# Kernel tuning notes

Measured on AMD Instinct MI355X. Metric: run time of the kernel, lower is better.

Reference implementation:

```python
import jax, jax.numpy as jnp
import numpy as np

B, C, H, W = 16, 64, 64, 64  # z_e shape; C == embedding_dim
K = 1024                     # num_embeddings
COMMITMENT_COST = 0.25
EPS = 1e-5


def setup_inputs() -> dict:
    key = jax.random.key(0)
    k1, k2 = jax.random.split(key)
    z_e = jax.random.normal(k1, (B, C, H, W), dtype=jnp.float32)
    # codebook init ~ U(-1/D, 1/D) as in the torch module
    emb_w = jax.random.uniform(k2, (K, C), dtype=jnp.float32, minval=-1.0 / C, maxval=1.0 / C)
    return {"z_e": z_e, "emb_w": emb_w}


def reference(z_e, emb_w):
    orig_dtype = z_e.dtype
    b, c, h, w = z_e.shape
    z = z_e.astype(jnp.float32)
    # per-channel std over (batch, h, w); computed under no_grad in torch -> stop_gradient
    std = jax.lax.stop_gradient(
        jnp.clip(jnp.std(z, axis=(0, 2, 3), keepdims=True, ddof=1), EPS, None)
    )
    z = z / std                                        # [b,c,h,w]
    zf = z.transpose(0, 2, 3, 1).reshape(-1, c)        # [N, c]
    ew = emb_w.astype(jnp.float32)                     # [K, c]
    # squared euclidean distances: ||z||^2 - 2 z.e + ||e||^2  -> [N, K]
    d = (
        jnp.sum(zf * zf, axis=1, keepdims=True)
        - 2.0 * (zf @ ew.T)
        + jnp.sum(ew * ew, axis=1)
    )
    idx = jnp.argmin(d, axis=1)                        # [N]
    z_q = ew[idx].reshape(b, h, w, c).transpose(0, 3, 1, 2)  # [b,c,h,w]
    z_sg = jax.lax.stop_gradient(z)
    commitment = COMMITMENT_COST * jnp.mean((z_sg - z_q) ** 2)
    codebook = jnp.mean((z_sg - z_q) ** 2)             # eval-mode codebook loss
    vq_loss = commitment + codebook
    z_q_st = (z + jax.lax.stop_gradient(z_q - z)).astype(orig_dtype)
    n_tokens = idx.shape[0]
    counts = jnp.zeros((K,), dtype=jnp.float32).at[idx].add(1.0)
    avg_probs = counts / n_tokens
    perplexity = jnp.exp(-jnp.sum(avg_probs * jnp.log(jnp.clip(avg_probs, 1e-10, None))))
    indices = idx.reshape(b, h, w)
    return z_q_st, vq_loss, perplexity, indices
```

## Files before the change

kernel.cpp:

```cpp
#include <hip/hip_runtime.h>
#include <math.h>
#include <float.h>

#define HW 4096
#define CHW 262144
#define NTOK 65536
#define NELEM 4194304

#define WS_LOSS 0
#define WS_STD  512
#define WS_EE   576
#define WS_ETG  1600

__device__ __forceinline__ void gload_lds16(const float* g, float* l) {
  __builtin_amdgcn_global_load_lds(
      (const __attribute__((address_space(1))) unsigned int*)g,
      (__attribute__((address_space(3))) unsigned int*)l, 16, 0, 0);
}

__global__ __launch_bounds__(1024) void k_pre(const float* __restrict__ z,
                                              const float* __restrict__ emb,
                                              float* __restrict__ stdv,
                                              float* __restrict__ etg,
                                              float* __restrict__ eeg) {
  __shared__ double rs[16], rs2[16];
  __shared__ float T[64][65];
  int tid = threadIdx.x;
  int blk = blockIdx.x;
  if (blk < 64) {
    int c = blk;
    double s = 0.0, s2 = 0.0;
    const float* base = z + c * HW;
    #pragma unroll 4
    for (int jj = 0; jj < 16; ++jj) {
      int f = tid + (jj << 10);
      int b = f >> 10, off4 = f & 1023;
      float4 v = *(const float4*)(base + (size_t)b * CHW + (off4 << 2));
      s  += (double)v.x + (double)v.y + (double)v.z + (double)v.w;
      s2 += (double)v.x * v.x + (double)v.y * v.y + (double)v.z * v.z + (double)v.w * v.w;
    }
    for (int o = 32; o > 0; o >>= 1) {
      s += __shfl_down(s, o, 64);
      s2 += __shfl_down(s2, o, 64);
    }
    int wv = tid >> 6, ln = tid & 63;
    if (ln == 0) { rs[wv] = s; rs2[wv] = s2; }
    __syncthreads();
    if (tid == 0) {
      double S = 0.0, S2 = 0.0;
      #pragma unroll
      for (int w = 0; w < 16; ++w) { S += rs[w]; S2 += rs2[w]; }
      const double N = (double)NTOK;
      double var = (S2 - S * S / N) / (N - 1.0);
      float sd = (float)sqrt(var);
      stdv[c] = fmaxf(sd, 1e-5f);
    }
  } else {
    int k0 = (blk - 64) << 6;
    {
      int code = tid >> 4, c4 = tid & 15;
      float4 v = *(const float4*)(emb + (size_t)((k0 + code) << 6) + (c4 << 2));
      T[code][(c4 << 2) + 0] = v.x;
      T[code][(c4 << 2) + 1] = v.y;
      T[code][(c4 << 2) + 2] = v.z;
      T[code][(c4 << 2) + 3] = v.w;
    }
    __syncthreads();
    {
      int c = tid >> 4, k4 = tid & 15;
      float4 v = make_float4(T[(k4 << 2) + 0][c], T[(k4 << 2) + 1][c],
                             T[(k4 << 2) + 2][c], T[(k4 << 2) + 3][c]);
      *(float4*)(etg + c * 1024 + k0 + (k4 << 2)) = v;
    }
    if (tid < 64) {
      const float* er = emb + (size_t)((k0 + tid) << 6);
      float s = 0.f;
      #pragma unroll
      for (int c = 0; c < 64; ++c) s = fmaf(er[c], er[c], s);
      eeg[k0 + tid] = s;
    }
  }
}

#define FMA8(ii, zc) \
  acc[ii].x = fmaf(zc, ea.x, acc[ii].x); \
  acc[ii].y = fmaf(zc, ea.y, acc[ii].y); \
  acc[ii].z = fmaf(zc, ea.z, acc[ii].z); \
  acc[ii].w = fmaf(zc, ea.w, acc[ii].w);

__global__ __launch_bounds__(256, 3) void k_vq(
    const float* __restrict__ z_e, const float* __restrict__ emb,
    const float* __restrict__ stdv, const float* __restrict__ eeg,
    const float* __restrict__ etg,
    float* __restrict__ out_zq, float* __restrict__ out_idx,
    float* __restrict__ loss_part) {
  __shared__ float zt[64 * 128];
  __shared__ float et[64 * 64];
  __shared__ float eetS[64];
  __shared__ float zzt[128];
  __shared__ float sstd[64];
  __shared__ float rbd[2 * 128];
  __shared__ int   rbk[2 * 128];
  __shared__ int   skf[128];
  __shared__ float sred[4];

  int tid = threadIdx.x;
  int lane = tid & 63;
  int wv = tid >> 6;
  int blk = blockIdx.x;
  int b = blk >> 5;
  int s0 = (blk & 31) << 7;

  if (tid < 64) sstd[tid] = stdv[tid];
  __syncthreads();

  const float* zbase = z_e + (size_t)b * CHW + s0;
  #pragma unroll
  for (int jj = 0; jj < 8; ++jj) {
    int f = tid + (jj << 8);
    int c = f >> 5, t4 = f & 31;
    float4 v = *(const float4*)(zbase + (size_t)c * HW + (t4 << 2));
    float sd = sstd[c];
    v.x /= sd; v.y /= sd; v.z /= sd; v.w /= sd;
    *(float4*)&zt[(c << 7) + (t4 << 2)] = v;
  }
  __syncthreads();

  if (tid < 128) {
    float a = 0.f;
    #pragma unroll
    for (int c = 0; c < 64; ++c) { float v = zt[(c << 7) + tid]; a = fmaf(v, v, a); }
    zzt[tid] = a;
  }
  __syncthreads();

  int toff = ((wv >> 1) << 6) + ((lane >> 3) << 3);
  int kloc = ((wv & 1) << 5) + ((lane & 7) << 2);
  int tq4 = toff >> 2;
  int kq4 = kloc >> 2;

  float zzr[8];
  #pragma unroll
  for (int ii = 0; ii < 8; ++ii) zzr[ii] = zzt[toff + ii];

  float bd[8]; int bk[8];
  #pragma unroll
  for (int ii = 0; ii < 8; ++ii) { bd[ii] = FLT_MAX; bk[ii] = 0; }

  int c0 = tid >> 4;
  int k16 = (tid & 15) << 2;
  const float* gbase = etg + c0 * 1024 + k16;
  float* lbase = et + (c0 << 6) + k16;

  for (int tile = 0; tile < 16; ++tile) {
    __syncthreads();
    {
      const float* gsrc = gbase + (tile << 6);
      #pragma unroll
      for (int jj = 0; jj < 4; ++jj)
        gload_lds16(gsrc + jj * 16384, lbase + jj * 1024);
      if (tid < 64) eetS[tid] = eeg[(tile << 6) + tid];
    }
    __syncthreads();

    float4 acc[8];
    #pragma unroll
    for (int ii = 0; ii < 8; ++ii) acc[ii] = make_float4(0.f, 0.f, 0.f, 0.f);

    #pragma unroll 8
    for (int c = 0; c < 64; ++c) {
      float4 ea = ((const float4*)et)[(c << 4) + kq4];
      float4 za = ((const float4*)zt)[(c << 5) + tq4];
      float4 zb = ((const float4*)zt)[(c << 5) + tq4 + 1];
      FMA8(0, za.x) FMA8(1, za.y) FMA8(2, za.z) FMA8(3, za.w)
      FMA8(4, zb.x) FMA8(5, zb.y) FMA8(6, zb.z) FMA8(7, zb.w)
    }

    int kb = (tile << 6) + kloc;
    float e0 = eetS[kloc], e1 = eetS[kloc + 1];
    float e2 = eetS[kloc + 2], e3 = eetS[kloc + 3];
    #pragma unroll
    for (int ii = 0; ii < 8; ++ii) {
      float z2 = zzr[ii];
      float dd0 = (z2 - 2.0f * acc[ii].x) + e0;
      float dd1 = (z2 - 2.0f * acc[ii].y) + e1;
      float dd2 = (z2 - 2.0f * acc[ii].z) + e2;
      float dd3 = (z2 - 2.0f * acc[ii].w) + e3;
      if (dd0 < bd[ii]) { bd[ii] = dd0; bk[ii] = kb; }
      if (dd1 < bd[ii]) { bd[ii] = dd1; bk[ii] = kb + 1; }
      if (dd2 < bd[ii]) { bd[ii] = dd2; bk[ii] = kb + 2; }
      if (dd3 < bd[ii]) { bd[ii] = dd3; bk[ii] = kb + 3; }
    }
  }

  #pragma unroll
  for (int m = 1; m <= 4; m <<= 1) {
    #pragma unroll
    for (int ii = 0; ii < 8; ++ii) {
      float od = __shfl_xor(bd[ii], m, 64);
      int   ok = __shfl_xor(bk[ii], m, 64);
      if (od < bd[ii] || (od == bd[ii] && ok < bk[ii])) { bd[ii] = od; bk[ii] = ok; }
    }
  }
  if ((lane & 7) == 0) {
    int base = ((wv & 1) << 7) + toff;
    #pragma unroll
    for (int ii = 0; ii < 8; ++ii) { rbd[base + ii] = bd[ii]; rbk[base + ii] = bk[ii]; }
  }
  __syncthreads();

  if (tid < 128) {
    float d0 = rbd[tid];       int k0 = rbk[tid];
    float d1 = rbd[128 + tid]; int k1 = rbk[128 + tid];
    int kb2 = (d1 < d0 || (d1 == d0 && k1 < k0)) ? k1 : k0;
    skf[tid] = kb2;
    out_idx[(blk << 7) + tid] = (float)kb2;
  }
  __syncthreads();

  int t = tid & 127;
  int ch = tid >> 7;
  int kq = skf[t];
  const float* eq = emb + (size_t)(kq << 6) + (ch << 5);
  float lsum = 0.f;
  float* ob = out_zq + (size_t)b * CHW + s0 + t;
  #pragma unroll
  for (int jj = 0; jj < 32; ++jj) {
    int c = (ch << 5) + jj;
    float zv = zt[(c << 7) + t];
    float e = eq[jj];
    float df = zv - e;
    lsum = fmaf(df, df, lsum);
    ob[(size_t)c * HW] = zv + (e - zv);
  }
  for (int o = 32; o > 0; o >>= 1) lsum += __shfl_down(lsum, o, 64);
  if (lane == 0) sred[wv] = lsum;
  __syncthreads();
  if (tid == 0) loss_part[blk] = sred[0] + sred[1] + sred[2] + sred[3];
}

__global__ __launch_bounds__(1024) void k_post(const float* __restrict__ loss_part,
                                               const float* __restrict__ out_idx,
                                               float* __restrict__ out_scalars) {
  __shared__ int hist[1024];
  __shared__ double rl[16], rh[16];
  int tid = threadIdx.x;
  hist[tid] = 0;
  __syncthreads();
  const float2* idx2 = (const float2*)out_idx;
  #pragma unroll
  for (int jj = 0; jj < 32; ++jj) {
    float2 v = idx2[tid + (jj << 10)];
    atomicAdd(&hist[(int)v.x], 1);
    atomicAdd(&hist[(int)v.y], 1);
  }
  __syncthreads();
  double ls = 0.0;
  if (tid < 512) ls = (double)loss_part[tid];
  float p = (float)hist[tid] * (1.0f / 65536.0f);
  float lg = logf(fmaxf(p, 1e-10f));
  double hs = (double)(p * lg);
  for (int o = 32; o > 0; o >>= 1) {
    ls += __shfl_down(ls, o, 64);
    hs += __shfl_down(hs, o, 64);
  }
  int wv = tid >> 6, ln = tid & 63;
  if (ln == 0) { rl[wv] = ls; rh[wv] = hs; }
  __syncthreads();
  if (tid == 0) {
    double L = 0.0, Hn = 0.0;
    #pragma unroll
    for (int w = 0; w < 16; ++w) { L += rl[w]; Hn += rh[w]; }
    float m = (float)(L / (double)NELEM);
    out_scalars[0] = 0.25f * m + m;
    out_scalars[1] = expf((float)(-Hn));
  }
}

extern "C" void kernel_launch(void* const* d_in, const int* in_sizes, int n_in,
                              void* d_out, int out_size, void* d_ws, size_t ws_size,
                              hipStream_t stream) {
  const float* z_e = (const float*)d_in[0];
  const float* emb = (const float*)d_in[1];
  float* ws = (float*)d_ws;
  float* loss_part = ws + WS_LOSS;
  float* stdv = ws + WS_STD;
  float* eeg = ws + WS_EE;
  float* etg = ws + WS_ETG;

  float* out = (float*)d_out;
  float* out_zq = out;
  float* out_scalars = out + NELEM;
  float* out_idx = out + NELEM + 2;

  k_pre<<<80, 1024, 0, stream>>>(z_e, emb, stdv, etg, eeg);
  k_vq<<<512, 256, 0, stream>>>(z_e, emb, stdv, eeg, etg, out_zq, out_idx, loss_part);
  k_post<<<1, 1024, 0, stream>>>(loss_part, out_idx, out_scalars);
}
```

Measured before the change: 206.6 us.

## Read codebook directly from global memory and fuse post-reduction into last block

The distance loop no longer stages codebook tiles in LDS with barriers. Each thread now reads 8 codebook columns straight from global/L2 memory and keeps 64 accumulators over 8 passes. The separate single-block post kernel is removed: the last VQ block to finish, detected with a global atomic counter, builds the histogram and writes the loss and perplexity scalars. This removes per-tile barriers and one kernel launch, but it adds register pressure and uncached global reads in the inner loop, and the final reduction now runs with only 256 threads.

```diff
diff --git a/kernel.cpp b/kernel.cpp
--- a/kernel.cpp
+++ b/kernel.cpp
@@ -11,22 +11,19 @@
 #define WS_STD  512
 #define WS_EE   576
 #define WS_ETG  1600
-
-__device__ __forceinline__ void gload_lds16(const float* g, float* l) {
-  __builtin_amdgcn_global_load_lds(
-      (const __attribute__((address_space(1))) unsigned int*)g,
-      (__attribute__((address_space(3))) unsigned int*)l, 16, 0, 0);
-}
+#define WS_DONE 67136
 
 __global__ __launch_bounds__(1024) void k_pre(const float* __restrict__ z,
                                               const float* __restrict__ emb,
                                               float* __restrict__ stdv,
                                               float* __restrict__ etg,
-                                              float* __restrict__ eeg) {
+                                              float* __restrict__ eeg,
+                                              int* __restrict__ done) {
   __shared__ double rs[16], rs2[16];
   __shared__ float T[64][65];
   int tid = threadIdx.x;
   int blk = blockIdx.x;
+  if (blk == 0 && tid == 0) *done = 0;
   if (blk < 64) {
     int c = blk;
     double s = 0.0, s2 = 0.0;
@@ -82,27 +79,33 @@
   }
 }
 
-#define FMA8(ii, zc) \
-  acc[ii].x = fmaf(zc, ea.x, acc[ii].x); \
-  acc[ii].y = fmaf(zc, ea.y, acc[ii].y); \
-  acc[ii].z = fmaf(zc, ea.z, acc[ii].z); \
-  acc[ii].w = fmaf(zc, ea.w, acc[ii].w);
+#define STEP8(i, zc) \
+  acc0[i].x = fmaf(zc, ea.x, acc0[i].x); \
+  acc0[i].y = fmaf(zc, ea.y, acc0[i].y); \
+  acc0[i].z = fmaf(zc, ea.z, acc0[i].z); \
+  acc0[i].w = fmaf(zc, ea.w, acc0[i].w); \
+  acc1[i].x = fmaf(zc, eb.x, acc1[i].x); \
+  acc1[i].y = fmaf(zc, eb.y, acc1[i].y); \
+  acc1[i].z = fmaf(zc, eb.z, acc1[i].z); \
+  acc1[i].w = fmaf(zc, eb.w, acc1[i].w);
 
 __global__ __launch_bounds__(256, 3) void k_vq(
     const float* __restrict__ z_e, const float* __restrict__ emb,
     const float* __restrict__ stdv, const float* __restrict__ eeg,
     const float* __restrict__ etg,
     float* __restrict__ out_zq, float* __restrict__ out_idx,
-    float* __restrict__ loss_part) {
+    float* __restrict__ loss_part, int* __restrict__ done,
+    float* __restrict__ out_scalars) {
   __shared__ float zt[64 * 128];
-  __shared__ float et[64 * 64];
-  __shared__ float eetS[64];
   __shared__ float zzt[128];
   __shared__ float sstd[64];
-  __shared__ float rbd[2 * 128];
-  __shared__ int   rbk[2 * 128];
+  __shared__ float rbd[2][128];
+  __shared__ int   rbk[2][128];
   __shared__ int   skf[128];
   __shared__ float sred[4];
+  __shared__ int   hist[1024];
+  __shared__ int   lastFlag;
+  __shared__ double rl[4], rh[4];
 
   int tid = threadIdx.x;
   int lane = tid & 63;
@@ -134,62 +137,54 @@
   }
   __syncthreads();
 
-  int toff = ((wv >> 1) << 6) + ((lane >> 3) << 3);
-  int kloc = ((wv & 1) << 5) + ((lane & 7) << 2);
-  int tq4 = toff >> 2;
-  int kq4 = kloc >> 2;
+  int tg = lane >> 3, cg = lane & 7;
+  int wt = wv >> 1, wc = wv & 1;
+  int tbase = wt * 64 + tg * 8;
+  const float4* zp = (const float4*)&zt[tbase];
 
   float zzr[8];
   #pragma unroll
-  for (int ii = 0; ii < 8; ++ii) zzr[ii] = zzt[toff + ii];
+  for (int ii = 0; ii < 8; ++ii) zzr[ii] = zzt[tbase + ii];
 
   float bd[8]; int bk[8];
   #pragma unroll
   for (int ii = 0; ii < 8; ++ii) { bd[ii] = FLT_MAX; bk[ii] = 0; }
 
-  int c0 = tid >> 4;
-  int k16 = (tid & 15) << 2;
-  const float* gbase = etg + c0 * 1024 + k16;
-  float* lbase = et + (c0 << 6) + k16;
-
-  for (int tile = 0; tile < 16; ++tile) {
-    __syncthreads();
-    {
-      const float* gsrc = gbase + (tile << 6);
-      #pragma unroll
-      for (int jj = 0; jj < 4; ++jj)
-        gload_lds16(gsrc + jj * 16384, lbase + jj * 1024);
-      if (tid < 64) eetS[tid] = eeg[(tile << 6) + tid];
-    }
-    __syncthreads();
-
-    float4 acc[8];
-    #pragma unroll
-    for (int ii = 0; ii < 8; ++ii) acc[ii] = make_float4(0.f, 0.f, 0.f, 0.f);
-
-    #pragma unroll 8
+  for (int pass = 0; pass < 8; ++pass) {
+    int kk = (pass << 7) + (wc << 6) + (cg << 3);
+    const float* ep = etg + kk;
+
+    float4 acc0[8], acc1[8];
+    #pragma unroll
+    for (int ii = 0; ii < 8; ++ii) {
+      acc0[ii] = make_float4(0.f, 0.f, 0.f, 0.f);
+      acc1[ii] = make_float4(0.f, 0.f, 0.f, 0.f);
+    }
+
+    #pragma unroll 4
     for (int c = 0; c < 64; ++c) {
-      float4 ea = ((const float4*)et)[(c << 4) + kq4];
-      float4 za = ((const float4*)zt)[(c << 5) + tq4];
-      float4 zb = ((const float4*)zt)[(c << 5) + tq4 + 1];
-      FMA8(0, za.x) FMA8(1, za.y) FMA8(2, za.z) FMA8(3, za.w)
-      FMA8(4, zb.x) FMA8(5, zb.y) FMA8(6, zb.z) FMA8(7, zb.w)
-    }
-
-    int kb = (tile << 6) + kloc;
-    float e0 = eetS[kloc], e1 = eetS[kloc + 1];
-    float e2 = eetS[kloc + 2], e3 = eetS[kloc + 3];
+      float4 ea = *(const float4*)ep;
+      float4 eb = *(const float4*)(ep + 4);
+      float4 za = zp[c << 5];
+      float4 zb = zp[(c << 5) + 1];
+      STEP8(0, za.x) STEP8(1, za.y) STEP8(2, za.z) STEP8(3, za.w)
+      STEP8(4, zb.x) STEP8(5, zb.y) STEP8(6, zb.z) STEP8(7, zb.w)
+      ep += 1024;
+    }
+
+    float4 eea = *(const float4*)(eeg + kk);
+    float4 eeb = *(const float4*)(eeg + kk + 4);
+    float eev[8] = {eea.x, eea.y, eea.z, eea.w, eeb.x, eeb.y, eeb.z, eeb.w};
     #pragma unroll
     for (int ii = 0; ii < 8; ++ii) {
       float z2 = zzr[ii];
-      float dd0 = (z2 - 2.0f * acc[ii].x) + e0;
-      float dd1 = (z2 - 2.0f * acc[ii].y) + e1;
-      float dd2 = (z2 - 2.0f * acc[ii].z) + e2;
-      float dd3 = (z2 - 2.0f * acc[ii].w) + e3;
-      if (dd0 < bd[ii]) { bd[ii] = dd0; bk[ii] = kb; }
-      if (dd1 < bd[ii]) { bd[ii] = dd1; bk[ii] = kb + 1; }
-      if (dd2 < bd[ii]) { bd[ii] = dd2; bk[ii] = kb + 2; }
-      if (dd3 < bd[ii]) { bd[ii] = dd3; bk[ii] = kb + 3; }
+      float av[8] = {acc0[ii].x, acc0[ii].y, acc0[ii].z, acc0[ii].w,
+                     acc1[ii].x, acc1[ii].y, acc1[ii].z, acc1[ii].w};
+      #pragma unroll
+      for (int jj = 0; jj < 8; ++jj) {
+        float dd = (z2 - 2.0f * av[jj]) + eev[jj];
+        if (dd < bd[ii]) { bd[ii] = dd; bk[ii] = kk + jj; }
+      }
     }
   }
 
@@ -202,75 +197,80 @@
       if (od < bd[ii] || (od == bd[ii] && ok < bk[ii])) { bd[ii] = od; bk[ii] = ok; }
     }
   }
-  if ((lane & 7) == 0) {
-    int base = ((wv & 1) << 7) + toff;
-    #pragma unroll
-    for (int ii = 0; ii < 8; ++ii) { rbd[base + ii] = bd[ii]; rbk[base + ii] = bk[ii]; }
+  if (cg == 0) {
+    #pragma unroll
+    for (int ii = 0; ii < 8; ++ii) { rbd[wc][tbase + ii] = bd[ii]; rbk[wc][tbase + ii] = bk[ii]; }
   }
   __syncthreads();
 
   if (tid < 128) {
-    float d0 = rbd[tid];       int k0 = rbk[tid];
-    float d1 = rbd[128 + tid]; int k1 = rbk[128 + tid];
+    float d0 = rbd[0][tid]; int k0 = rbk[0][tid];
+    float d1 = rbd[1][tid]; int k1 = rbk[1][tid];
     int kb2 = (d1 < d0 || (d1 == d0 && k1 < k0)) ? k1 : k0;
     skf[tid] = kb2;
     out_idx[(blk << 7) + tid] = (float)kb2;
   }
   __syncthreads();
 
-  int t = tid & 127;
-  int ch = tid >> 7;
-  int kq = skf[t];
-  const float* eq = emb + (size_t)(kq << 6) + (ch << 5);
-  float lsum = 0.f;
-  float* ob = out_zq + (size_t)b * CHW + s0 + t;
-  #pragma unroll
-  for (int jj = 0; jj < 32; ++jj) {
-    int c = (ch << 5) + jj;
-    float zv = zt[(c << 7) + t];
-    float e = eq[jj];
-    float df = zv - e;
-    lsum = fmaf(df, df, lsum);
-    ob[(size_t)c * HW] = zv + (e - zv);
-  }
-  for (int o = 32; o > 0; o >>= 1) lsum += __shfl_down(lsum, o, 64);
-  if (lane == 0) sred[wv] = lsum;
-  __syncthreads();
-  if (tid == 0) loss_part[blk] = sred[0] + sred[1] + sred[2] + sred[3];
-}
-
-__global__ __launch_bounds__(1024) void k_post(const float* __restrict__ loss_part,
-                                               const float* __restrict__ out_idx,
-                                               float* __restrict__ out_scalars) {
-  __shared__ int hist[1024];
-  __shared__ double rl[16], rh[16];
-  int tid = threadIdx.x;
-  hist[tid] = 0;
-  __syncthreads();
-  const float2* idx2 = (const float2*)out_idx;
-  #pragma unroll
-  for (int jj = 0; jj < 32; ++jj) {
-    float2 v = idx2[tid + (jj << 10)];
-    atomicAdd(&hist[(int)v.x], 1);
-    atomicAdd(&hist[(int)v.y], 1);
-  }
-  __syncthreads();
-  double ls = 0.0;
-  if (tid < 512) ls = (double)loss_part[tid];
-  float p = (float)hist[tid] * (1.0f / 65536.0f);
-  float lg = logf(fmaxf(p, 1e-10f));
-  double hs = (double)(p * lg);
+  {
+    int t = tid & 127;
+    int ch = tid >> 7;
+    int kq = skf[t];
+    const float* eq = emb + (size_t)(kq << 6) + (ch << 5);
+    float lsum = 0.f;
+    float* ob = out_zq + (size_t)b * CHW + s0 + t;
+    #pragma unroll
+    for (int jj = 0; jj < 32; ++jj) {
+      int c = (ch << 5) + jj;
+      float zv = zt[(c << 7) + t];
+      float e = eq[jj];
+      float df = zv - e;
+      lsum = fmaf(df, df, lsum);
+      ob[(size_t)c * HW] = zv + (e - zv);
+    }
+    for (int o = 32; o > 0; o >>= 1) lsum += __shfl_down(lsum, o, 64);
+    if (lane == 0) sred[wv] = lsum;
+  }
+  __syncthreads();
+
+  if (tid == 0) {
+    loss_part[blk] = sred[0] + sred[1] + sred[2] + sred[3];
+    __threadfence();
+    int prev = atomicAdd(done, 1);
+    lastFlag = (prev == 511);
+  }
+  __syncthreads();
+  if (!lastFlag) return;
+
+  #pragma unroll
+  for (int jj = 0; jj < 4; ++jj) hist[tid + (jj << 8)] = 0;
+  __syncthreads();
+  {
+    const float2* idx2 = (const float2*)out_idx;
+    for (int i = tid; i < NTOK / 2; i += 256) {
+      float2 v = idx2[i];
+      atomicAdd(&hist[(int)v.x], 1);
+      atomicAdd(&hist[(int)v.y], 1);
+    }
+  }
+  __syncthreads();
+  double ls = (double)loss_part[tid] + (double)loss_part[tid + 256];
+  double hs = 0.0;
+  #pragma unroll
+  for (int jj = 0; jj < 4; ++jj) {
+    float p = (float)hist[tid + (jj << 8)] * (1.0f / 65536.0f);
+    float lg = logf(fmaxf(p, 1e-10f));
+    hs += (double)(p * lg);
+  }
   for (int o = 32; o > 0; o >>= 1) {
     ls += __shfl_down(ls, o, 64);
     hs += __shfl_down(hs, o, 64);
   }
-  int wv = tid >> 6, ln = tid & 63;
-  if (ln == 0) { rl[wv] = ls; rh[wv] = hs; }
+  if (lane == 0) { rl[wv] = ls; rh[wv] = hs; }
   __syncthreads();
   if (tid == 0) {
-    double L = 0.0, Hn = 0.0;
-    #pragma unroll
-    for (int w = 0; w < 16; ++w) { L += rl[w]; Hn += rh[w]; }
+    double L = rl[0] + rl[1] + rl[2] + rl[3];
+    double Hn = rh[0] + rh[1] + rh[2] + rh[3];
     float m = (float)(L / (double)NELEM);
     out_scalars[0] = 0.25f * m + m;
     out_scalars[1] = expf((float)(-Hn));
@@ -287,13 +287,14 @@
   float* stdv = ws + WS_STD;
   float* eeg = ws + WS_EE;
   float* etg = ws + WS_ETG;
+  int* done = (int*)(ws + WS_DONE);
 
   float* out = (float*)d_out;
   float* out_zq = out;
   float* out_scalars = out + NELEM;
   float* out_idx = out + NELEM + 2;
 
-  k_pre<<<80, 1024, 0, stream>>>(z_e, emb, stdv, etg, eeg);
-  k_vq<<<512, 256, 0, stream>>>(z_e, emb, stdv, eeg, etg, out_zq, out_idx, loss_part);
-  k_post<<<1, 1024, 0, stream>>>(loss_part, out_idx, out_scalars);
+  k_pre<<<80, 1024, 0, stream>>>(z_e, emb, stdv, etg, eeg, done);
+  k_vq<<<512, 256, 0, stream>>>(z_e, emb, stdv, eeg, etg, out_zq, out_idx,
+                                loss_part, done, out_scalars);
 }
```

Result: slower. 299.9 us (+45.2%).

## Compute VQ distances with split-bf16 MFMA and exact fp32 fallback for near-ties

Applied to the files above, without the earlier changes.

Replaces the fp32 FMA distance GEMM with bf16 MFMA, splitting each value into high and low bf16 parts so three cross products approximate fp32 accuracy. Each token tracks its best and second-best distance, and tokens whose margin falls below a threshold are recomputed exactly in fp32 against the full codebook. The z tile is no longer kept as fp32 in LDS, so the output stage re-reads z_e from global memory. This trades extra global reads, fallback work and lower occupancy (launch bounds 3 to 2) for much higher matrix throughput.

```diff
diff --git a/kernel.cpp b/kernel.cpp
--- a/kernel.cpp
+++ b/kernel.cpp
@@ -10,21 +10,28 @@
 #define WS_LOSS 0
 #define WS_STD  512
 #define WS_EE   576
-#define WS_ETG  1600
-
-__device__ __forceinline__ void gload_lds16(const float* g, float* l) {
-  __builtin_amdgcn_global_load_lds(
-      (const __attribute__((address_space(1))) unsigned int*)g,
-      (__attribute__((address_space(3))) unsigned int*)l, 16, 0, 0);
+#define WS_E2   1600
+
+#define EPSM 2.0e-3f
+
+typedef __attribute__((ext_vector_type(8))) short bf16x8;
+typedef __attribute__((ext_vector_type(4))) float f32x4;
+
+__device__ __forceinline__ unsigned short f2bf(float x) {
+  unsigned u = __float_as_uint(x);
+  u += 0x7FFFu + ((u >> 16) & 1u);
+  return (unsigned short)(u >> 16);
+}
+__device__ __forceinline__ float bf2f(unsigned short h) {
+  return __uint_as_float(((unsigned)h) << 16);
 }
 
 __global__ __launch_bounds__(1024) void k_pre(const float* __restrict__ z,
                                               const float* __restrict__ emb,
                                               float* __restrict__ stdv,
-                                              float* __restrict__ etg,
+                                              unsigned short* __restrict__ e2g,
                                               float* __restrict__ eeg) {
   __shared__ double rs[16], rs2[16];
-  __shared__ float T[64][65];
   int tid = threadIdx.x;
   int blk = blockIdx.x;
   if (blk < 64) {
@@ -60,17 +67,14 @@
     {
       int code = tid >> 4, c4 = tid & 15;
       float4 v = *(const float4*)(emb + (size_t)((k0 + code) << 6) + (c4 << 2));
-      T[code][(c4 << 2) + 0] = v.x;
-      T[code][(c4 << 2) + 1] = v.y;
-      T[code][(c4 << 2) + 2] = v.z;
-      T[code][(c4 << 2) + 3] = v.w;
-    }
-    __syncthreads();
-    {
-      int c = tid >> 4, k4 = tid & 15;
-      float4 v = make_float4(T[(k4 << 2) + 0][c], T[(k4 << 2) + 1][c],
-                             T[(k4 << 2) + 2][c], T[(k4 << 2) + 3][c]);
-      *(float4*)(etg + c * 1024 + k0 + (k4 << 2)) = v;
+      unsigned short h0 = f2bf(v.x), h1 = f2bf(v.y), h2 = f2bf(v.z), h3 = f2bf(v.w);
+      unsigned short l0 = f2bf(v.x - bf2f(h0)), l1 = f2bf(v.y - bf2f(h1));
+      unsigned short l2 = f2bf(v.z - bf2f(h2)), l3 = f2bf(v.w - bf2f(h3));
+      unsigned short* row = e2g + (size_t)(k0 + code) * 128;
+      *(uint2*)(row + (c4 << 2)) =
+          make_uint2((unsigned)h0 | ((unsigned)h1 << 16), (unsigned)h2 | ((unsigned)h3 << 16));
+      *(uint2*)(row + 64 + (c4 << 2)) =
+          make_uint2((unsigned)l0 | ((unsigned)l1 << 16), (unsigned)l2 | ((unsigned)l3 << 16));
     }
     if (tid < 64) {
       const float* er = emb + (size_t)((k0 + tid) << 6);
@@ -82,26 +86,22 @@
   }
 }
 
-#define FMA8(ii, zc) \
-  acc[ii].x = fmaf(zc, ea.x, acc[ii].x); \
-  acc[ii].y = fmaf(zc, ea.y, acc[ii].y); \
-  acc[ii].z = fmaf(zc, ea.z, acc[ii].z); \
-  acc[ii].w = fmaf(zc, ea.w, acc[ii].w);
-
-__global__ __launch_bounds__(256, 3) void k_vq(
+__global__ __launch_bounds__(256, 2) void k_vq(
     const float* __restrict__ z_e, const float* __restrict__ emb,
     const float* __restrict__ stdv, const float* __restrict__ eeg,
-    const float* __restrict__ etg,
+    const unsigned short* __restrict__ e2g,
     float* __restrict__ out_zq, float* __restrict__ out_idx,
     float* __restrict__ loss_part) {
-  __shared__ float zt[64 * 128];
-  __shared__ float et[64 * 64];
-  __shared__ float eetS[64];
-  __shared__ float zzt[128];
+  __shared__ unsigned short Abuf[128 * 136];
+  __shared__ unsigned short Bt[128 * 136];
+  __shared__ float eeS[1024];
   __shared__ float sstd[64];
-  __shared__ float rbd[2 * 128];
-  __shared__ int   rbk[2 * 128];
+  __shared__ float mbd[2][128];
+  __shared__ float msec[2][128];
+  __shared__ int   mbk[2][128];
   __shared__ int   skf[128];
+  __shared__ int   ambList[128];
+  __shared__ int   ambN;
   __shared__ float sred[4];
 
   int tid = threadIdx.x;
@@ -112,129 +112,188 @@
   int s0 = (blk & 31) << 7;
 
   if (tid < 64) sstd[tid] = stdv[tid];
-  __syncthreads();
-
-  const float* zbase = z_e + (size_t)b * CHW + s0;
   #pragma unroll
-  for (int jj = 0; jj < 8; ++jj) {
-    int f = tid + (jj << 8);
-    int c = f >> 5, t4 = f & 31;
-    float4 v = *(const float4*)(zbase + (size_t)c * HW + (t4 << 2));
-    float sd = sstd[c];
-    v.x /= sd; v.y /= sd; v.z /= sd; v.w /= sd;
-    *(float4*)&zt[(c << 7) + (t4 << 2)] = v;
-  }
-  __syncthreads();
-
-  if (tid < 128) {
-    float a = 0.f;
-    #pragma unroll
-    for (int c = 0; c < 64; ++c) { float v = zt[(c << 7) + tid]; a = fmaf(v, v, a); }
-    zzt[tid] = a;
-  }
-  __syncthreads();
-
-  int toff = ((wv >> 1) << 6) + ((lane >> 3) << 3);
-  int kloc = ((wv & 1) << 5) + ((lane & 7) << 2);
-  int tq4 = toff >> 2;
-  int kq4 = kloc >> 2;
-
-  float zzr[8];
+  for (int j = 0; j < 4; ++j) eeS[tid + (j << 8)] = eeg[tid + (j << 8)];
+  if (tid == 0) ambN = 0;
+  __syncthreads();
+
+  {
+    int tok = tid & 127, sect = tid >> 7;
+    const float* zsrc = z_e + (size_t)b * CHW + (size_t)(sect << 5) * HW + s0 + tok;
+    unsigned hw[16], lw[16];
+    #pragma unroll
+    for (int cc = 0; cc < 32; ++cc) {
+      float v = zsrc[(size_t)cc * HW] / sstd[(sect << 5) + cc];
+      unsigned short h = f2bf(v);
+      unsigned short l = f2bf(v - bf2f(h));
+      if (cc & 1) { hw[cc >> 1] |= ((unsigned)h) << 16; lw[cc >> 1] |= ((unsigned)l) << 16; }
+      else        { hw[cc >> 1] = h;                    lw[cc >> 1] = l; }
+    }
+    unsigned short* arow = Abuf + tok * 136;
+    #pragma unroll
+    for (int q = 0; q < 4; ++q) {
+      *(uint4*)(arow + (sect << 5) + (q << 3)) =
+          make_uint4(hw[4 * q], hw[4 * q + 1], hw[4 * q + 2], hw[4 * q + 3]);
+      *(uint4*)(arow + 64 + (sect << 5) + (q << 3)) =
+          make_uint4(lw[4 * q], lw[4 * q + 1], lw[4 * q + 2], lw[4 * q + 3]);
+    }
+  }
+
+  int quad = lane >> 4, l15 = lane & 15;
+  int wt = wv >> 1, wc = wv & 1;
+
+  float bd[16], sec[16];
+  int bk[16];
   #pragma unroll
-  for (int ii = 0; ii < 8; ++ii) zzr[ii] = zzt[toff + ii];
-
-  float bd[8]; int bk[8];
-  #pragma unroll
-  for (int ii = 0; ii < 8; ++ii) { bd[ii] = FLT_MAX; bk[ii] = 0; }
-
-  int c0 = tid >> 4;
-  int k16 = (tid & 15) << 2;
-  const float* gbase = etg + c0 * 1024 + k16;
-  float* lbase = et + (c0 << 6) + k16;
-
-  for (int tile = 0; tile < 16; ++tile) {
+  for (int i = 0; i < 16; ++i) { bd[i] = FLT_MAX; sec[i] = FLT_MAX; bk[i] = 0; }
+
+  for (int ct = 0; ct < 8; ++ct) {
     __syncthreads();
     {
-      const float* gsrc = gbase + (tile << 6);
-      #pragma unroll
-      for (int jj = 0; jj < 4; ++jj)
-        gload_lds16(gsrc + jj * 16384, lbase + jj * 1024);
-      if (tid < 64) eetS[tid] = eeg[(tile << 6) + tid];
+      int code = tid >> 1, part = tid & 1;
+      const uint4* src = (const uint4*)(e2g + ((size_t)((ct << 7) + code) << 7) + (part << 6));
+      uint4* dst = (uint4*)(Bt + code * 136 + (part << 6));
+      #pragma unroll
+      for (int j = 0; j < 8; ++j) dst[j] = src[j];
     }
     __syncthreads();
 
-    float4 acc[8];
-    #pragma unroll
-    for (int ii = 0; ii < 8; ++ii) acc[ii] = make_float4(0.f, 0.f, 0.f, 0.f);
-
-    #pragma unroll 8
-    for (int c = 0; c < 64; ++c) {
-      float4 ea = ((const float4*)et)[(c << 4) + kq4];
-      float4 za = ((const float4*)zt)[(c << 5) + tq4];
-      float4 zb = ((const float4*)zt)[(c << 5) + tq4 + 1];
-      FMA8(0, za.x) FMA8(1, za.y) FMA8(2, za.z) FMA8(3, za.w)
-      FMA8(4, zb.x) FMA8(5, zb.y) FMA8(6, zb.z) FMA8(7, zb.w)
-    }
-
-    int kb = (tile << 6) + kloc;
-    float e0 = eetS[kloc], e1 = eetS[kloc + 1];
-    float e2 = eetS[kloc + 2], e3 = eetS[kloc + 3];
-    #pragma unroll
-    for (int ii = 0; ii < 8; ++ii) {
-      float z2 = zzr[ii];
-      float dd0 = (z2 - 2.0f * acc[ii].x) + e0;
-      float dd1 = (z2 - 2.0f * acc[ii].y) + e1;
-      float dd2 = (z2 - 2.0f * acc[ii].z) + e2;
-      float dd3 = (z2 - 2.0f * acc[ii].w) + e3;
-      if (dd0 < bd[ii]) { bd[ii] = dd0; bk[ii] = kb; }
-      if (dd1 < bd[ii]) { bd[ii] = dd1; bk[ii] = kb + 1; }
-      if (dd2 < bd[ii]) { bd[ii] = dd2; bk[ii] = kb + 2; }
-      if (dd3 < bd[ii]) { bd[ii] = dd3; bk[ii] = kb + 3; }
+    f32x4 acc[4][4];
+    #pragma unroll
+    for (int mt = 0; mt < 4; ++mt)
+      #pragma unroll
+      for (int nt = 0; nt < 4; ++nt) acc[mt][nt] = (f32x4)(0.f);
+
+    const int aoffs[6] = {0, 32, 64, 96, 0, 32};
+    const int boffs[6] = {0, 32, 0, 32, 64, 96};
+    #pragma unroll
+    for (int s = 0; s < 6; ++s) {
+      bf16x8 af[4], bfr[4];
+      #pragma unroll
+      for (int mt = 0; mt < 4; ++mt)
+        af[mt] = *(const bf16x8*)(Abuf + ((wt << 6) + (mt << 4) + l15) * 136 + aoffs[s] + (quad << 3));
+      #pragma unroll
+      for (int nt = 0; nt < 4; ++nt)
+        bfr[nt] = *(const bf16x8*)(Bt + ((wc << 6) + (nt << 4) + l15) * 136 + boffs[s] + (quad << 3));
+      #pragma unroll
+      for (int mt = 0; mt < 4; ++mt)
+        #pragma unroll
+        for (int nt = 0; nt < 4; ++nt)
+          acc[mt][nt] = __builtin_amdgcn_mfma_f32_16x16x32_bf16(af[mt], bfr[nt], acc[mt][nt], 0, 0, 0);
+    }
+
+    int kbase = (ct << 7) + (wc << 6);
+    #pragma unroll
+    for (int nt = 0; nt < 4; ++nt) {
+      int kcode = kbase + (nt << 4) + l15;
+      float eev = eeS[kcode];
+      #pragma unroll
+      for (int mt = 0; mt < 4; ++mt) {
+        #pragma unroll
+        for (int r = 0; r < 4; ++r) {
+          float sv = fmaf(-2.0f, acc[mt][nt][r], eev);
+          int slot = (mt << 2) + r;
+          if (sv < bd[slot]) { sec[slot] = bd[slot]; bd[slot] = sv; bk[slot] = kcode; }
+          else if (sv < sec[slot]) { sec[slot] = sv; }
+        }
+      }
     }
   }
 
   #pragma unroll
-  for (int m = 1; m <= 4; m <<= 1) {
-    #pragma unroll
-    for (int ii = 0; ii < 8; ++ii) {
-      float od = __shfl_xor(bd[ii], m, 64);
-      int   ok = __shfl_xor(bk[ii], m, 64);
-      if (od < bd[ii] || (od == bd[ii] && ok < bk[ii])) { bd[ii] = od; bk[ii] = ok; }
-    }
-  }
-  if ((lane & 7) == 0) {
-    int base = ((wv & 1) << 7) + toff;
-    #pragma unroll
-    for (int ii = 0; ii < 8; ++ii) { rbd[base + ii] = bd[ii]; rbk[base + ii] = bk[ii]; }
+  for (int m = 1; m <= 8; m <<= 1) {
+    #pragma unroll
+    for (int slot = 0; slot < 16; ++slot) {
+      float obd = __shfl_xor(bd[slot], m, 64);
+      int   obk = __shfl_xor(bk[slot], m, 64);
+      float osec = __shfl_xor(sec[slot], m, 64);
+      if (obd < bd[slot] || (obd == bd[slot] && obk < bk[slot])) {
+        sec[slot] = fminf(bd[slot], osec); bd[slot] = obd; bk[slot] = obk;
+      } else {
+        sec[slot] = fminf(sec[slot], obd);
+      }
+    }
+  }
+  if (l15 == 0) {
+    #pragma unroll
+    for (int mt = 0; mt < 4; ++mt)
+      #pragma unroll
+      for (int r = 0; r < 4; ++r) {
+        int t = (wt << 6) + (mt << 4) + (quad << 2) + r;
+        int slot = (mt << 2) + r;
+        mbd[wc][t] = bd[slot]; mbk[wc][t] = bk[slot]; msec[wc][t] = sec[slot];
+      }
   }
   __syncthreads();
 
   if (tid < 128) {
-    float d0 = rbd[tid];       int k0 = rbk[tid];
-    float d1 = rbd[128 + tid]; int k1 = rbk[128 + tid];
-    int kb2 = (d1 < d0 || (d1 == d0 && k1 < k0)) ? k1 : k0;
-    skf[tid] = kb2;
-    out_idx[(blk << 7) + tid] = (float)kb2;
-  }
-  __syncthreads();
-
-  int t = tid & 127;
-  int ch = tid >> 7;
-  int kq = skf[t];
-  const float* eq = emb + (size_t)(kq << 6) + (ch << 5);
-  float lsum = 0.f;
-  float* ob = out_zq + (size_t)b * CHW + s0 + t;
-  #pragma unroll
-  for (int jj = 0; jj < 32; ++jj) {
-    int c = (ch << 5) + jj;
-    float zv = zt[(c << 7) + t];
-    float e = eq[jj];
-    float df = zv - e;
-    lsum = fmaf(df, df, lsum);
-    ob[(size_t)c * HW] = zv + (e - zv);
-  }
-  for (int o = 32; o > 0; o >>= 1) lsum += __shfl_down(lsum, o, 64);
-  if (lane == 0) sred[wv] = lsum;
+    float b0 = mbd[0][tid], b1 = mbd[1][tid];
+    int k0 = mbk[0][tid], k1 = mbk[1][tid];
+    float fbd, fsec; int fbk;
+    if (b1 < b0 || (b1 == b0 && k1 < k0)) { fbd = b1; fbk = k1; fsec = fminf(b0, msec[1][tid]); }
+    else                                  { fbd = b0; fbk = k0; fsec = fminf(msec[0][tid], b1); }
+    skf[tid] = fbk;
+    if (fsec - fbd <= EPSM) { int p = atomicAdd(&ambN, 1); ambList[p] = tid; }
+  }
+  __syncthreads();
+
+  {
+    int na = ambN;
+    for (int i = wv; i < na; i += 4) {
+      int t = ambList[i];
+      float zvl = z_e[(size_t)b * CHW + (size_t)lane * HW + s0 + t] / sstd[lane];
+      float zz = 0.f;
+      #pragma unroll
+      for (int c = 0; c < 64; ++c) { float zc = __shfl(zvl, c, 64); zz = fmaf(zc, zc, zz); }
+      float bdl = FLT_MAX; int bkl = 0;
+      for (int kk = 0; kk < 16; ++kk) {
+        int k = (lane << 4) + kk;
+        const float* er = emb + ((size_t)k << 6);
+        float dot = 0.f;
+        #pragma unroll
+        for (int c4 = 0; c4 < 16; ++c4) {
+          float4 ev = *(const float4*)(er + (c4 << 2));
+          dot = fmaf(ev.x, __shfl(zvl, (c4 << 2) + 0, 64), dot);
+          dot = fmaf(ev.y, __shfl(zvl, (c4 << 2) + 1, 64), dot);
+          dot = fmaf(ev.z, __shfl(zvl, (c4 << 2) + 2, 64), dot);
+          dot = fmaf(ev.w, __shfl(zvl, (c4 << 2) + 3, 64), dot);
+        }
+        float dd = (zz - 2.0f * dot) + eeS[k];
+        if (dd < bdl) { bdl = dd; bkl = k; }
+      }
+      #pragma unroll
+      for (int m = 1; m <= 32; m <<= 1) {
+        float od = __shfl_xor(bdl, m, 64);
+        int   ok = __shfl_xor(bkl, m, 64);
+        if (od < bdl || (od == bdl && ok < bkl)) { bdl = od; bkl = ok; }
+      }
+      if (lane == 0) skf[t] = bkl;
+    }
+  }
+  __syncthreads();
+
+  if (tid < 128) out_idx[(blk << 7) + tid] = (float)skf[tid];
+
+  {
+    int t = tid & 127;
+    int ch = tid >> 7;
+    int kq = skf[t];
+    const float* eq = emb + ((size_t)kq << 6) + (ch << 5);
+    const float* zb2 = z_e + (size_t)b * CHW + s0 + t;
+    float* ob = out_zq + (size_t)b * CHW + s0 + t;
+    float lsum = 0.f;
+    #pragma unroll
+    for (int jj = 0; jj < 32; ++jj) {
+      int c = (ch << 5) + jj;
+      float zv = zb2[(size_t)c * HW] / sstd[c];
+      float e = eq[jj];
+      float df = zv - e;
+      lsum = fmaf(df, df, lsum);
+      ob[(size_t)c * HW] = zv + (e - zv);
+    }
+    for (int o = 32; o > 0; o >>= 1) lsum += __shfl_down(lsum, o, 64);
+    if (lane == 0) sred[wv] = lsum;
+  }
   __syncthreads();
   if (tid == 0) loss_part[blk] = sred[0] + sred[1] + sred[2] + sred[3];
 }
@@ -286,14 +345,14 @@
   float* loss_part = ws + WS_LOSS;
   float* stdv = ws + WS_STD;
   float* eeg = ws + WS_EE;
-  float* etg = ws + WS_ETG;
+  unsigned short* e2g = (unsigned short*)(ws + WS_E2);
 
   float* out = (float*)d_out;
   float* out_zq = out;
   float* out_scalars = out + NELEM;
   float* out_idx = out + NELEM + 2;
 
-  k_pre<<<80, 1024, 0, stream>>>(z_e, emb, stdv, etg, eeg);
-  k_vq<<<512, 256, 0, stream>>>(z_e, emb, stdv, eeg, etg, out_zq, out_idx, loss_part);
+  k_pre<<<80, 1024, 0, stream>>>(z_e, emb, stdv, e2g, eeg);
+  k_vq<<<512, 256, 0, stream>>>(z_e, emb, stdv, eeg, e2g, out_zq, out_idx, loss_part);
   k_post<<<1, 1024, 0, stream>>>(loss_part, out_idx, out_scalars);
 }
```

New measurement: 320.6 us. 1.55x slower.
